# Optimization experiments

Hardware: AMD Instinct MI355X
Metric: run time of the kernel (lower is better)

The kernel has to match this reference:

```python
import jax, jax.numpy as jnp
import numpy as np

B, T, V, E, H = 64, 512, 50000, 256, 512
UNK_IDX = 1


def setup_inputs() -> dict:
    key = jax.random.key(0)
    ks = jax.random.split(key, 12)
    ids = jax.random.randint(ks[0], (B, T), 0, V)
    unk_mask = jax.random.uniform(ks[1], (B, T)) < 0.05
    enc_input = jnp.where(unk_mask, UNK_IDX, ids)
    lens = jnp.sort(jax.random.randint(ks[2], (B,), 256, T + 1))[::-1]
    seq_lens = lens.at[0].set(T)
    u = lambda k, sh: jax.random.uniform(k, sh, jnp.float32, -0.02, 0.02)
    emb_table = jax.random.normal(ks[3], (V, E), jnp.float32) * 0.1
    # torch gate order i,f,g,o; bias = b_ih + b_hh with forget-gate slice = 1.0 each -> 2.0 combined
    def bias(k):
        b = jnp.zeros((4 * H,), jnp.float32)
        return b.at[H:2 * H].set(2.0)
    return {
        "enc_input": enc_input,
        "seq_lens": seq_lens,
        "emb_table": emb_table,
        "Wih_f": u(ks[4], (4 * H, E)), "Whh_f": u(ks[5], (4 * H, H)), "b_f": bias(ks[6]),
        "Wih_b": u(ks[7], (4 * H, E)), "Whh_b": u(ks[8], (4 * H, H)), "b_b": bias(ks[9]),
        "Wp": u(ks[10], (E, 2 * H)) * 2.0, "bp": jnp.zeros((E,), jnp.float32),
    }


def _lstm_dir(x, mask, Wih, Whh, b, reverse):
    # x: [T,B,D], mask: [T,B] bool. Packed-sequence semantics: state frozen and
    # output zeroed at padded steps; reverse scan starts at t=len-1 per sequence.
    Bsz = x.shape[1]
    h0 = jnp.zeros((Bsz, H), x.dtype)
    c0 = jnp.zeros((Bsz, H), x.dtype)

    def step(carry, inp):
        h, c = carry
        x_t, m = inp
        g = x_t @ Wih.T + h @ Whh.T + b
        i, f, gg, o = jnp.split(g, 4, axis=-1)
        c_new = jax.nn.sigmoid(f) * c + jax.nn.sigmoid(i) * jnp.tanh(gg)
        h_new = jax.nn.sigmoid(o) * jnp.tanh(c_new)
        mm = m[:, None]
        h = jnp.where(mm, h_new, h)
        c = jnp.where(mm, c_new, c)
        return (h, c), jnp.where(mm, h_new, 0.0)

    (hT, cT), outs = jax.lax.scan(step, (h0, c0), (x, mask), reverse=reverse)
    return outs, hT, cT


def _bilstm(embedded, mask_tb, Wih_f, Whh_f, b_f, Wih_b, Whh_b, b_b):
    x = jnp.swapaxes(embedded, 0, 1)  # [T,B,E]
    of, hf, cf = _lstm_dir(x, mask_tb, Wih_f, Whh_f, b_f, reverse=False)
    ob, hb, cb = _lstm_dir(x, mask_tb, Wih_b, Whh_b, b_b, reverse=True)
    h = jnp.swapaxes(jnp.concatenate([of, ob], axis=-1), 0, 1)  # [B,T,2H]
    h_n = jnp.stack([hf, hb])  # [2,B,H]
    c_n = jnp.stack([cf, cb])
    return h, h_n, c_n


def reference(enc_input, seq_lens, emb_table, Wih_f, Whh_f, b_f, Wih_b, Whh_b, b_b, Wp, bp):
    valid = jnp.arange(T)[None, :] < seq_lens[:, None]  # [B,T]
    mask_tb = valid.T  # [T,B]
    embedded = emb_table[enc_input]  # [B,T,E]
    h, h_n, c_n = _bilstm(embedded, mask_tb, Wih_f, Whh_f, b_f, Wih_b, Whh_b, b_b)

    # vectorized OOV branch: replace UNK embeddings with proj of neighbor states
    is_unk = (enc_input == UNK_IDX) & valid  # [B,T]
    fwd_ctx = jnp.pad(h[:, :-1, :H], ((0, 0), (1, 0), (0, 0)))  # h[i,j-1,:H], 0 at j=0
    next_valid = (jnp.arange(T)[None, :] + 1) < seq_lens[:, None]
    bwd_ctx = jnp.pad(h[:, 1:, H:], ((0, 0), (0, 1), (0, 0))) * next_valid[..., None]
    unk_emb = jnp.concatenate([fwd_ctx, bwd_ctx], axis=-1)  # [B,T,2H]
    new_emb = unk_emb @ Wp.T + bp  # [B,T,E]
    embedded = jnp.where(is_unk[..., None], new_emb, embedded)

    h, h_n, c_n = _bilstm(embedded, mask_tb, Wih_f, Whh_f, b_f, Wih_b, Whh_b, b_b)
    return h, h_n, c_n
```

## Files before the change

kernel.cpp:

```cpp
#include <hip/hip_runtime.h>
#include <hip/hip_bf16.h>
#include <stdint.h>

typedef __attribute__((ext_vector_type(8))) short short8;
typedef __attribute__((ext_vector_type(4))) float f32x4;
typedef __attribute__((ext_vector_type(4))) unsigned int u32x4;

static __device__ __forceinline__ unsigned short f2b(float x) {
  union { float f; unsigned u; } v; v.f = x;
  unsigned r = (v.u + 0x7FFFu + ((v.u >> 16) & 1u)) >> 16;
  return (unsigned short)r;
}
static __device__ __forceinline__ float sigm(float x) { return 1.0f / (1.0f + __expf(-x)); }
static __device__ __forceinline__ float tanh_(float x) { return 2.0f / (1.0f + __expf(-2.0f * x)) - 1.0f; }

#define WS_EMB   0u
#define WS_WHH   16777216u
#define WS_WIH   20971520u
#define WS_WPB   23068672u
#define WS_SYNC  23592960u
#define WS_HEXS1 (WS_SYNC + 0u)
#define WS_HEXS2 (WS_SYNC + 262144u)
#define WS_HEXF1 (WS_SYNC + 524288u)
#define WS_HEXF2 (WS_SYNC + 786432u)
#define WS_CNTS1 (WS_SYNC + 1048576u)
#define WS_CNTS2 (WS_SYNC + 1052672u)
#define WS_CNTF1 (WS_SYNC + 1056768u)
#define WS_CNTF2 (WS_SYNC + 1060864u)
#define WS_REG1  (WS_SYNC + 1064960u)
#define WS_REG2  (WS_SYNC + 1065472u)
#define WS_SYNC_SPAN 1065984u

__global__ void prep(const float* __restrict__ wihf, const float* __restrict__ whhf,
                     const float* __restrict__ wihb, const float* __restrict__ whhb,
                     const float* __restrict__ wp,
                     unsigned short* __restrict__ wih_bf, unsigned short* __restrict__ whh_bf,
                     unsigned short* __restrict__ wp_bf) {
  int i = blockIdx.x * 256 + threadIdx.x;
  int stride = gridDim.x * 256;
  for (int k = i; k < 2048 * 512; k += stride) { whh_bf[k] = f2b(whhf[k]); whh_bf[2048 * 512 + k] = f2b(whhb[k]); }
  for (int k = i; k < 2048 * 256; k += stride) { wih_bf[k] = f2b(wihf[k]); wih_bf[2048 * 256 + k] = f2b(wihb[k]); }
  for (int k = i; k < 256 * 1024; k += stride) { wp_bf[k] = f2b(wp[k]); }
}

__global__ void gather(const int* __restrict__ enc, const float* __restrict__ tab,
                       unsigned short* __restrict__ emb) {
  for (int tok = blockIdx.x; tok < 64 * 512; tok += gridDim.x) {
    int b = tok >> 9, t = tok & 511;
    int id = enc[tok];
    int e = threadIdx.x;
    emb[(size_t)(t * 64 + b) * 256 + e] = f2b(tab[(size_t)id * 256 + e]);
  }
}

template<int FAST>
static __device__ __forceinline__ void lstm_body(
    int d, int q, int g,
    const unsigned short* __restrict__ emb,
    const unsigned short* __restrict__ whh,
    const unsigned short* __restrict__ wih,
    const float* __restrict__ bf_, const float* __restrict__ bb_,
    const int* __restrict__ lens,
    char* __restrict__ hexS, char* __restrict__ hexF,
    unsigned int* __restrict__ myc,
    float* __restrict__ out_h, float* __restrict__ out_hn, float* __restrict__ out_cn,
    unsigned short* lds_h, float (*gbuf)[16][17], unsigned short (*hnew)[16])
{
  const int tid = threadIdx.x;
  const int wv = tid >> 6, lane = tid & 63;
  const int l15 = lane & 15, lhi = lane >> 4;

  short8 Bh[16], Bx[8];
  {
    const int row = wv * 512 + g * 16 + l15;
    const unsigned short* pw = whh + ((size_t)d * 2048 + row) * 512 + lhi * 8;
#pragma unroll
    for (int kk = 0; kk < 16; ++kk) Bh[kk] = *(const short8*)(pw + kk * 32);
    const unsigned short* px = wih + ((size_t)d * 2048 + row) * 256 + lhi * 8;
#pragma unroll
    for (int kk = 0; kk < 8; ++kk) Bx[kk] = *(const short8*)(px + kk * 32);
  }
  const float bias = (d ? bb_ : bf_)[wv * 512 + g * 16 + l15];

  const int cb = tid & 15, ch = tid >> 4;
  const int gb = q * 16 + cb;
  const int mylen = lens[gb];
  float c_st = 0.f, h_cy = 0.f;

  char* hexG = FAST ? (hexF + (d * 4 + q) * 32768) : hexS;

  for (int s = 0; s < 512; ++s) {
    const int t = d ? (511 - s) : s;
    const int p = s & 1;

    f32x4 acc0 = { bias, bias, bias, bias };
    f32x4 acc1 = { 0.f, 0.f, 0.f, 0.f };
    {
      const unsigned short* xa = emb + ((size_t)(t * 64 + q * 16 + l15)) * 256 + lhi * 8;
#pragma unroll
      for (int kk = 0; kk < 8; ++kk) {
        short8 a = *(const short8*)(xa + kk * 32);
        acc0 = __builtin_amdgcn_mfma_f32_16x16x32_bf16(a, Bx[kk], acc0, 0, 0, 0);
      }
    }

    if (s > 0) {
      const unsigned int tgt = 32u * (unsigned)s;
      if (lane == 0) {
        if (FAST) {
          for (;;) {
            unsigned c;
            asm volatile("global_load_dword %0, %1, off sc0\n\ts_waitcnt vmcnt(0)"
                         : "=v"(c) : "v"(myc) : "memory");
            if (c >= tgt) break;
            __builtin_amdgcn_s_sleep(1);
          }
        } else {
          while (__hip_atomic_load(myc, __ATOMIC_RELAXED, __HIP_MEMORY_SCOPE_AGENT) < tgt)
            __builtin_amdgcn_s_sleep(1);
        }
      }
    }

    u32x4 hv0, hv1, hv2, hv3;
    {
      const char* src = FAST
          ? hexG + p * 16384 + (tid & 15) * 1024 + (tid >> 4) * 64
          : hexG + ((size_t)(p * 2 + d) * 64 + q * 16 + (tid & 15)) * 1024 + (tid >> 4) * 64;
      if (FAST) {
        asm volatile(
          "global_load_dwordx4 %0, %4, off sc0\n\t"
          "global_load_dwordx4 %1, %4, off offset:16 sc0\n\t"
          "global_load_dwordx4 %2, %4, off offset:32 sc0\n\t"
          "global_load_dwordx4 %3, %4, off offset:48 sc0\n\t"
          "s_waitcnt vmcnt(0)"
          : "=&v"(hv0), "=&v"(hv1), "=&v"(hv2), "=&v"(hv3) : "v"(src) : "memory");
      } else {
        asm volatile(
          "global_load_dwordx4 %0, %4, off sc0 sc1\n\t"
          "global_load_dwordx4 %1, %4, off offset:16 sc0 sc1\n\t"
          "global_load_dwordx4 %2, %4, off offset:32 sc0 sc1\n\t"
          "global_load_dwordx4 %3, %4, off offset:48 sc0 sc1\n\t"
          "s_waitcnt vmcnt(0)"
          : "=&v"(hv0), "=&v"(hv1), "=&v"(hv2), "=&v"(hv3) : "v"(src) : "memory");
      }
    }
    __syncthreads();
    {
      const int row = tid & 15;
      const int qt = tid >> 4;
      const int swz = (row & 7) << 4;
      char* base = (char*)lds_h + row * 1024;
      *(u32x4*)(base + ((qt * 64 +  0) ^ swz)) = hv0;
      *(u32x4*)(base + ((qt * 64 + 16) ^ swz)) = hv1;
      *(u32x4*)(base + ((qt * 64 + 32) ^ swz)) = hv2;
      *(u32x4*)(base + ((qt * 64 + 48) ^ swz)) = hv3;
    }
    __syncthreads();

    {
      const int rb0 = l15 * 1024 + lhi * 16;
      const int swz = (l15 & 7) << 4;
#pragma unroll
      for (int kk = 0; kk < 16; kk += 2) {
        short8 a0 = *(const short8*)((const char*)lds_h + ((rb0 + kk * 64) ^ swz));
        short8 a1 = *(const short8*)((const char*)lds_h + ((rb0 + (kk + 1) * 64) ^ swz));
        acc0 = __builtin_amdgcn_mfma_f32_16x16x32_bf16(a0, Bh[kk], acc0, 0, 0, 0);
        acc1 = __builtin_amdgcn_mfma_f32_16x16x32_bf16(a1, Bh[kk + 1], acc1, 0, 0, 0);
      }
    }
    f32x4 acc = acc0 + acc1;

#pragma unroll
    for (int r = 0; r < 4; ++r) gbuf[wv][l15][lhi * 4 + r] = acc[r];
    __syncthreads();

    float hn_out; bool m;
    {
      float gi = gbuf[0][ch][cb], gf = gbuf[1][ch][cb], gg = gbuf[2][ch][cb], go = gbuf[3][ch][cb];
      float cn_ = sigm(gf) * c_st + sigm(gi) * tanh_(gg);
      float hn_ = sigm(go) * tanh_(cn_);
      m = (t < mylen);
      c_st = m ? cn_ : c_st;
      h_cy = m ? hn_ : h_cy;
      hn_out = m ? hn_ : 0.f;
      hnew[cb][ch] = f2b(h_cy);
    }
    __syncthreads();

    if (wv == 0) {
      unsigned long long v = ((const unsigned long long*)hnew)[lane];
      char* dst = FAST
          ? hexG + ((s + 1) & 1) * 16384 + (lane >> 2) * 1024 + g * 32 + (lane & 3) * 8
          : hexG + ((size_t)(((s + 1) & 1) * 2 + d) * 64 + q * 16 + (lane >> 2)) * 1024 + g * 32 + (lane & 3) * 8;
      if (FAST) {
        asm volatile("global_store_dwordx2 %0, %1, off sc0" :: "v"(dst), "v"(v) : "memory");
        asm volatile("s_waitcnt vmcnt(0)" ::: "memory");
        if (lane == 0)
          __hip_atomic_fetch_add(myc, 1u, __ATOMIC_RELAXED, __HIP_MEMORY_SCOPE_WORKGROUP);
      } else {
        asm volatile("global_store_dwordx2 %0, %1, off sc0 sc1" :: "v"(dst), "v"(v) : "memory");
        asm volatile("s_waitcnt vmcnt(0)" ::: "memory");
        if (lane == 0)
          __hip_atomic_fetch_add(myc, 1u, __ATOMIC_RELAXED, __HIP_MEMORY_SCOPE_AGENT);
      }
    }

    out_h[((size_t)gb * 512 + t) * 1024 + d * 512 + g * 16 + ch] = hn_out;
    if (s == 511) {
      size_t o = ((size_t)d * 64 + gb) * 512 + g * 16 + ch;
      out_hn[o] = h_cy;
      out_cn[o] = c_st;
    }
  }
}

__global__ __launch_bounds__(256, 1) void lstm(
    const unsigned short* __restrict__ emb, const unsigned short* __restrict__ whh,
    const unsigned short* __restrict__ wih,
    const float* __restrict__ bf_, const float* __restrict__ bb_,
    const int* __restrict__ lens,
    char* __restrict__ hexS, char* __restrict__ hexF,
    unsigned int* __restrict__ cntS, unsigned int* __restrict__ cntF,
    unsigned int* __restrict__ reg,
    float* __restrict__ out_h, float* __restrict__ out_hn, float* __restrict__ out_cn)
{
  __shared__ __align__(16) unsigned short lds_h[16 * 512];
  __shared__ float gbuf[4][16][17];
  __shared__ __align__(8) unsigned short hnew[16][16];
  __shared__ int sh[4];

  const int tid = threadIdx.x;
  if (tid == 0) {
    unsigned xcd = 0;
    asm volatile("s_getreg_b32 %0, hwreg(HW_REG_XCC_ID)" : "=s"(xcd));
    xcd &= 7u;
    unsigned slot = __hip_atomic_fetch_add(&reg[xcd], 1u, __ATOMIC_RELAXED, __HIP_MEMORY_SCOPE_AGENT);
    unsigned v[8];
    for (;;) {
      unsigned sm = 0;
#pragma unroll
      for (int i = 0; i < 8; ++i) {
        v[i] = __hip_atomic_load(&reg[i], __ATOMIC_RELAXED, __HIP_MEMORY_SCOPE_AGENT);
        sm += v[i];
      }
      if (sm == 256u) break;
      __builtin_amdgcn_s_sleep(8);
    }
    bool clean = (slot < 32u);
    for (int i = 0; i < 8; ++i) clean = clean && (v[i] == 32u);
    if (clean) { sh[0] = 1; sh[1] = (int)(xcd >> 2); sh[2] = (int)(xcd & 3); sh[3] = (int)slot; }
    else {
      int bid = blockIdx.x;
      sh[0] = 0; sh[1] = bid >> 7; sh[2] = (bid >> 5) & 3; sh[3] = bid & 31;
    }
  }
  __syncthreads();
  const int fast = sh[0], d = sh[1], q = sh[2], g = sh[3];
  unsigned int* myc = (fast ? cntF : cntS) + (d * 4 + q) * 128;

  if (fast)
    lstm_body<1>(d, q, g, emb, whh, wih, bf_, bb_, lens, hexS, hexF, myc,
                 out_h, out_hn, out_cn, lds_h, gbuf, hnew);
  else
    lstm_body<0>(d, q, g, emb, whh, wih, bf_, bb_, lens, hexS, hexF, myc,
                 out_h, out_hn, out_cn, lds_h, gbuf, hnew);
}

__global__ __launch_bounds__(256, 1) void unkproj(
    const int* __restrict__ enc, const int* __restrict__ lens,
    const float* __restrict__ h1,
    const unsigned short* __restrict__ wpb,
    const float* __restrict__ bp,
    unsigned short* __restrict__ emb)
{
  const int base = blockIdx.x * 16;
  const int tid = threadIdx.x;
  const int wv = tid >> 6, lane = tid & 63;
  const int l15 = lane & 15, lhi = lane >> 4;

  const int tokA = base + l15;
  const int bA = tokA >> 9, tA = tokA & 511;
  const bool unkA = (enc[tokA] == 1) && (tA < lens[bA]);
  if (!__any(unkA)) return;

  const bool fok = (tA > 0), bok = (tA < 511);
  const float* fptr = h1 + ((size_t)bA * 512 + (fok ? tA - 1 : 0)) * 1024;
  const float* bptr = h1 + ((size_t)bA * 512 + (bok ? tA + 1 : 0)) * 1024 + 512;

  f32x4 acc[4] = { {0,0,0,0}, {0,0,0,0}, {0,0,0,0}, {0,0,0,0} };

#pragma unroll 4
  for (int kk = 0; kk < 16; ++kk) {
    const int k = kk * 32 + lhi * 8;
    short8 a;
    if (fok) {
      f32x4 lo = *(const f32x4*)(fptr + k);
      f32x4 hi = *(const f32x4*)(fptr + k + 4);
#pragma unroll
      for (int j = 0; j < 4; ++j) { a[j] = (short)f2b(lo[j]); a[4 + j] = (short)f2b(hi[j]); }
    } else {
      a = short8{0,0,0,0,0,0,0,0};
    }
#pragma unroll
    for (int nt = 0; nt < 4; ++nt) {
      short8 bf = *(const short8*)(wpb + (size_t)(wv * 64 + nt * 16 + l15) * 1024 + k);
      acc[nt] = __builtin_amdgcn_mfma_f32_16x16x32_bf16(a, bf, acc[nt], 0, 0, 0);
    }
  }
#pragma unroll 4
  for (int kk = 0; kk < 16; ++kk) {
    const int k = kk * 32 + lhi * 8;
    short8 a;
    if (bok) {
      f32x4 lo = *(const f32x4*)(bptr + k);
      f32x4 hi = *(const f32x4*)(bptr + k + 4);
#pragma unroll
      for (int j = 0; j < 4; ++j) { a[j] = (short)f2b(lo[j]); a[4 + j] = (short)f2b(hi[j]); }
    } else {
      a = short8{0,0,0,0,0,0,0,0};
    }
#pragma unroll
    for (int nt = 0; nt < 4; ++nt) {
      short8 bf = *(const short8*)(wpb + (size_t)(wv * 64 + nt * 16 + l15) * 1024 + 512 + k);
      acc[nt] = __builtin_amdgcn_mfma_f32_16x16x32_bf16(a, bf, acc[nt], 0, 0, 0);
    }
  }

#pragma unroll
  for (int r = 0; r < 4; ++r) {
    int tok = base + lhi * 4 + r;
    int b = tok >> 9, t = tok & 511;
    if (enc[tok] == 1 && t < lens[b]) {
#pragma unroll
      for (int nt = 0; nt < 4; ++nt) {
        int e = wv * 64 + nt * 16 + l15;
        emb[(size_t)(t * 64 + b) * 256 + e] = f2b(acc[nt][r] + bp[e]);
      }
    }
  }
}

extern "C" void kernel_launch(void* const* d_in, const int* in_sizes, int n_in,
                              void* d_out, int out_size, void* d_ws, size_t ws_size,
                              hipStream_t stream) {
  (void)in_sizes; (void)n_in; (void)out_size; (void)ws_size;
  const int*   enc  = (const int*)d_in[0];
  const int*   lens = (const int*)d_in[1];
  const float* tab  = (const float*)d_in[2];
  const float* wihf = (const float*)d_in[3];
  const float* whhf = (const float*)d_in[4];
  const float* bf_  = (const float*)d_in[5];
  const float* wihb = (const float*)d_in[6];
  const float* whhb = (const float*)d_in[7];
  const float* bb_  = (const float*)d_in[8];
  const float* wp   = (const float*)d_in[9];
  const float* bp   = (const float*)d_in[10];

  char* ws = (char*)d_ws;
  unsigned short* emb    = (unsigned short*)(ws + WS_EMB);
  unsigned short* whh_bf = (unsigned short*)(ws + WS_WHH);
  unsigned short* wih_bf = (unsigned short*)(ws + WS_WIH);
  unsigned short* wp_bf  = (unsigned short*)(ws + WS_WPB);

  float* out_h  = (float*)d_out;
  float* out_hn = out_h + (size_t)64 * 512 * 1024;
  float* out_cn = out_hn + 2 * 64 * 512;

  hipMemsetAsync(ws + WS_SYNC, 0, WS_SYNC_SPAN, stream);

  prep<<<2048, 256, 0, stream>>>(wihf, whhf, wihb, whhb, wp, wih_bf, whh_bf, wp_bf);
  gather<<<4096, 256, 0, stream>>>(enc, tab, emb);

  lstm<<<256, 256, 0, stream>>>(emb, whh_bf, wih_bf, bf_, bb_, lens,
                                ws + WS_HEXS1, ws + WS_HEXF1,
                                (unsigned int*)(ws + WS_CNTS1), (unsigned int*)(ws + WS_CNTF1),
                                (unsigned int*)(ws + WS_REG1),
                                out_h, out_hn, out_cn);
  unkproj<<<2048, 256, 0, stream>>>(enc, lens, out_h, wp_bf, bp, emb);
  lstm<<<256, 256, 0, stream>>>(emb, whh_bf, wih_bf, bf_, bb_, lens,
                                ws + WS_HEXS2, ws + WS_HEXF2,
                                (unsigned int*)(ws + WS_CNTS2), (unsigned int*)(ws + WS_CNTF2),
                                (unsigned int*)(ws + WS_REG2),
                                out_h, out_hn, out_cn);
}
```

Measured before the change: 3.414 ms.

## Halve LSTM block count, doubling hidden slice per block with per-block step flags

The persistent bidirectional LSTM kernel now runs 128 blocks of 512 threads, each owning 32 hidden units (8 waves), instead of 256 blocks of 256 threads with 16 units. The cross-block step barrier changes from an atomic counter to per-block step flags, which lanes poll in parallel with a wave-wide vote. Hidden-state exchange uses wider 16-byte stores and fewer loads per thread, and a watchdog limit is added to the spin loops. The aim is to cut the number of participants in each per-step global synchronisation and shorten the serial latency chain. In exchange each block does twice the MFMA work per step on a single CU, so per-step compute latency may grow.

```diff
diff --git a/kernel.cpp b/kernel.cpp
--- a/kernel.cpp
+++ b/kernel.cpp
@@ -19,17 +19,19 @@
 #define WS_WIH   20971520u
 #define WS_WPB   23068672u
 #define WS_SYNC  23592960u
-#define WS_HEXS1 (WS_SYNC + 0u)
-#define WS_HEXS2 (WS_SYNC + 262144u)
-#define WS_HEXF1 (WS_SYNC + 524288u)
-#define WS_HEXF2 (WS_SYNC + 786432u)
-#define WS_CNTS1 (WS_SYNC + 1048576u)
-#define WS_CNTS2 (WS_SYNC + 1052672u)
-#define WS_CNTF1 (WS_SYNC + 1056768u)
-#define WS_CNTF2 (WS_SYNC + 1060864u)
-#define WS_REG1  (WS_SYNC + 1064960u)
-#define WS_REG2  (WS_SYNC + 1065472u)
-#define WS_SYNC_SPAN 1065984u
+#define WS_HEXF1 (WS_SYNC + 0u)
+#define WS_HEXF2 (WS_SYNC + 262144u)
+#define WS_HEXS1 (WS_SYNC + 524288u)
+#define WS_HEXS2 (WS_SYNC + 786432u)
+#define WS_FLGF1 (WS_SYNC + 1048576u)
+#define WS_FLGF2 (WS_SYNC + 1049088u)
+#define WS_FLGS1 (WS_SYNC + 1049600u)
+#define WS_FLGS2 (WS_SYNC + 1050112u)
+#define WS_REG1  (WS_SYNC + 1050624u)
+#define WS_REG2  (WS_SYNC + 1051136u)
+#define WS_SYNC_SPAN 1051648u
+
+#define WD_LIMIT (1u << 17)
 
 __global__ void prep(const float* __restrict__ wihf, const float* __restrict__ whhf,
                      const float* __restrict__ wihb, const float* __restrict__ whhb,
@@ -61,18 +63,18 @@
     const unsigned short* __restrict__ wih,
     const float* __restrict__ bf_, const float* __restrict__ bb_,
     const int* __restrict__ lens,
-    char* __restrict__ hexS, char* __restrict__ hexF,
-    unsigned int* __restrict__ myc,
+    char* __restrict__ hexG, unsigned int* __restrict__ flg,
     float* __restrict__ out_h, float* __restrict__ out_hn, float* __restrict__ out_cn,
-    unsigned short* lds_h, float (*gbuf)[16][17], unsigned short (*hnew)[16])
+    unsigned short* lds_h, float (*gbuf)[32][17], unsigned short (*hnew)[40])
 {
   const int tid = threadIdx.x;
   const int wv = tid >> 6, lane = tid & 63;
   const int l15 = lane & 15, lhi = lane >> 4;
+  const int gt = wv >> 1, hs = wv & 1;
 
   short8 Bh[16], Bx[8];
+  const int row = gt * 512 + g * 32 + hs * 16 + l15;
   {
-    const int row = wv * 512 + g * 16 + l15;
     const unsigned short* pw = whh + ((size_t)d * 2048 + row) * 512 + lhi * 8;
 #pragma unroll
     for (int kk = 0; kk < 16; ++kk) Bh[kk] = *(const short8*)(pw + kk * 32);
@@ -80,15 +82,13 @@
 #pragma unroll
     for (int kk = 0; kk < 8; ++kk) Bx[kk] = *(const short8*)(px + kk * 32);
   }
-  const float bias = (d ? bb_ : bf_)[wv * 512 + g * 16 + l15];
+  const float bias = (d ? bb_ : bf_)[row];
 
   const int cb = tid & 15, ch = tid >> 4;
   const int gb = q * 16 + cb;
   const int mylen = lens[gb];
   float c_st = 0.f, h_cy = 0.f;
 
-  char* hexG = FAST ? (hexF + (d * 4 + q) * 32768) : hexS;
-
   for (int s = 0; s < 512; ++s) {
     const int t = d ? (511 - s) : s;
     const int p = s & 1;
@@ -105,56 +105,45 @@
     }
 
     if (s > 0) {
-      const unsigned int tgt = 32u * (unsigned)s;
-      if (lane == 0) {
-        if (FAST) {
-          for (;;) {
-            unsigned c;
-            asm volatile("global_load_dword %0, %1, off sc0\n\ts_waitcnt vmcnt(0)"
-                         : "=v"(c) : "v"(myc) : "memory");
-            if (c >= tgt) break;
-            __builtin_amdgcn_s_sleep(1);
-          }
-        } else {
-          while (__hip_atomic_load(myc, __ATOMIC_RELAXED, __HIP_MEMORY_SCOPE_AGENT) < tgt)
-            __builtin_amdgcn_s_sleep(1);
-        }
-      }
-    }
-
-    u32x4 hv0, hv1, hv2, hv3;
-    {
-      const char* src = FAST
-          ? hexG + p * 16384 + (tid & 15) * 1024 + (tid >> 4) * 64
-          : hexG + ((size_t)(p * 2 + d) * 64 + q * 16 + (tid & 15)) * 1024 + (tid >> 4) * 64;
-      if (FAST) {
+      const unsigned int tgt = (unsigned)s;
+      const unsigned int* fp = flg + (lane & 15);
+      for (unsigned it = 0;; ++it) {
+        unsigned f;
+        if (FAST)
+          asm volatile("global_load_dword %0, %1, off sc0\n\ts_waitcnt vmcnt(0)"
+                       : "=v"(f) : "v"(fp) : "memory");
+        else
+          asm volatile("global_load_dword %0, %1, off sc0 sc1\n\ts_waitcnt vmcnt(0)"
+                       : "=v"(f) : "v"(fp) : "memory");
+        if (__all((int)(f >= tgt))) break;
+        if (it > WD_LIMIT) break;
+        __builtin_amdgcn_s_sleep(1);
+      }
+    }
+
+    u32x4 hv0, hv1;
+    {
+      const char* src = hexG + p * 16384 + (tid >> 5) * 1024 + (tid & 31) * 32;
+      if (FAST)
         asm volatile(
-          "global_load_dwordx4 %0, %4, off sc0\n\t"
-          "global_load_dwordx4 %1, %4, off offset:16 sc0\n\t"
-          "global_load_dwordx4 %2, %4, off offset:32 sc0\n\t"
-          "global_load_dwordx4 %3, %4, off offset:48 sc0\n\t"
+          "global_load_dwordx4 %0, %2, off sc0\n\t"
+          "global_load_dwordx4 %1, %2, off offset:16 sc0\n\t"
           "s_waitcnt vmcnt(0)"
-          : "=&v"(hv0), "=&v"(hv1), "=&v"(hv2), "=&v"(hv3) : "v"(src) : "memory");
-      } else {
+          : "=&v"(hv0), "=&v"(hv1) : "v"(src) : "memory");
+      else
         asm volatile(
-          "global_load_dwordx4 %0, %4, off sc0 sc1\n\t"
-          "global_load_dwordx4 %1, %4, off offset:16 sc0 sc1\n\t"
-          "global_load_dwordx4 %2, %4, off offset:32 sc0 sc1\n\t"
-          "global_load_dwordx4 %3, %4, off offset:48 sc0 sc1\n\t"
+          "global_load_dwordx4 %0, %2, off sc0 sc1\n\t"
+          "global_load_dwordx4 %1, %2, off offset:16 sc0 sc1\n\t"
           "s_waitcnt vmcnt(0)"
-          : "=&v"(hv0), "=&v"(hv1), "=&v"(hv2), "=&v"(hv3) : "v"(src) : "memory");
-      }
-    }
-    __syncthreads();
-    {
-      const int row = tid & 15;
-      const int qt = tid >> 4;
-      const int swz = (row & 7) << 4;
-      char* base = (char*)lds_h + row * 1024;
-      *(u32x4*)(base + ((qt * 64 +  0) ^ swz)) = hv0;
-      *(u32x4*)(base + ((qt * 64 + 16) ^ swz)) = hv1;
-      *(u32x4*)(base + ((qt * 64 + 32) ^ swz)) = hv2;
-      *(u32x4*)(base + ((qt * 64 + 48) ^ swz)) = hv3;
+          : "=&v"(hv0), "=&v"(hv1) : "v"(src) : "memory");
+    }
+    {
+      const int row16 = tid >> 5;
+      const int off = (tid & 31) * 32;
+      const int swz = (row16 & 7) << 4;
+      char* base = (char*)lds_h + row16 * 1024;
+      *(u32x4*)(base + ((off) ^ swz)) = hv0;
+      *(u32x4*)(base + ((off + 16) ^ swz)) = hv1;
     }
     __syncthreads();
 
@@ -172,15 +161,15 @@
     f32x4 acc = acc0 + acc1;
 
 #pragma unroll
-    for (int r = 0; r < 4; ++r) gbuf[wv][l15][lhi * 4 + r] = acc[r];
+    for (int r = 0; r < 4; ++r) gbuf[gt][hs * 16 + l15][lhi * 4 + r] = acc[r];
     __syncthreads();
 
-    float hn_out; bool m;
+    float hn_out;
     {
       float gi = gbuf[0][ch][cb], gf = gbuf[1][ch][cb], gg = gbuf[2][ch][cb], go = gbuf[3][ch][cb];
       float cn_ = sigm(gf) * c_st + sigm(gi) * tanh_(gg);
       float hn_ = sigm(go) * tanh_(cn_);
-      m = (t < mylen);
+      bool m = (t < mylen);
       c_st = m ? cn_ : c_st;
       h_cy = m ? hn_ : h_cy;
       hn_out = m ? hn_ : 0.f;
@@ -189,45 +178,52 @@
     __syncthreads();
 
     if (wv == 0) {
-      unsigned long long v = ((const unsigned long long*)hnew)[lane];
-      char* dst = FAST
-          ? hexG + ((s + 1) & 1) * 16384 + (lane >> 2) * 1024 + g * 32 + (lane & 3) * 8
-          : hexG + ((size_t)(((s + 1) & 1) * 2 + d) * 64 + q * 16 + (lane >> 2)) * 1024 + g * 32 + (lane & 3) * 8;
+      const int prow = lane >> 2, c = lane & 3;
+      const char* hrow = (const char*)hnew + prow * 80 + c * 16;
+      unsigned long long a0 = *(const unsigned long long*)(hrow);
+      unsigned long long a1 = *(const unsigned long long*)(hrow + 8);
+      u32x4 v; v[0] = (unsigned)a0; v[1] = (unsigned)(a0 >> 32);
+      v[2] = (unsigned)a1; v[3] = (unsigned)(a1 >> 32);
+      char* dst = hexG + (p ^ 1) * 16384 + prow * 1024 + g * 64 + c * 16;
       if (FAST) {
-        asm volatile("global_store_dwordx2 %0, %1, off sc0" :: "v"(dst), "v"(v) : "memory");
-        asm volatile("s_waitcnt vmcnt(0)" ::: "memory");
-        if (lane == 0)
-          __hip_atomic_fetch_add(myc, 1u, __ATOMIC_RELAXED, __HIP_MEMORY_SCOPE_WORKGROUP);
+        asm volatile("global_store_dwordx4 %0, %1, off sc0\n\ts_waitcnt vmcnt(0)"
+                     :: "v"(dst), "v"(v) : "memory");
+        if (lane == 0) {
+          unsigned fv = (unsigned)(s + 1);
+          asm volatile("global_store_dword %0, %1, off sc0" :: "v"(flg + g), "v"(fv) : "memory");
+        }
       } else {
-        asm volatile("global_store_dwordx2 %0, %1, off sc0 sc1" :: "v"(dst), "v"(v) : "memory");
-        asm volatile("s_waitcnt vmcnt(0)" ::: "memory");
-        if (lane == 0)
-          __hip_atomic_fetch_add(myc, 1u, __ATOMIC_RELAXED, __HIP_MEMORY_SCOPE_AGENT);
-      }
-    }
-
-    out_h[((size_t)gb * 512 + t) * 1024 + d * 512 + g * 16 + ch] = hn_out;
+        asm volatile("global_store_dwordx4 %0, %1, off sc0 sc1\n\ts_waitcnt vmcnt(0)"
+                     :: "v"(dst), "v"(v) : "memory");
+        if (lane == 0) {
+          unsigned fv = (unsigned)(s + 1);
+          asm volatile("global_store_dword %0, %1, off sc0 sc1" :: "v"(flg + g), "v"(fv) : "memory");
+        }
+      }
+    }
+
+    out_h[((size_t)gb * 512 + t) * 1024 + d * 512 + g * 32 + ch] = hn_out;
     if (s == 511) {
-      size_t o = ((size_t)d * 64 + gb) * 512 + g * 16 + ch;
+      size_t o = ((size_t)d * 64 + gb) * 512 + g * 32 + ch;
       out_hn[o] = h_cy;
       out_cn[o] = c_st;
     }
   }
 }
 
-__global__ __launch_bounds__(256, 1) void lstm(
+__global__ __launch_bounds__(512, 1) void lstm(
     const unsigned short* __restrict__ emb, const unsigned short* __restrict__ whh,
     const unsigned short* __restrict__ wih,
     const float* __restrict__ bf_, const float* __restrict__ bb_,
     const int* __restrict__ lens,
-    char* __restrict__ hexS, char* __restrict__ hexF,
-    unsigned int* __restrict__ cntS, unsigned int* __restrict__ cntF,
+    char* __restrict__ hexF, char* __restrict__ hexS,
+    unsigned int* __restrict__ flgF, unsigned int* __restrict__ flgS,
     unsigned int* __restrict__ reg,
     float* __restrict__ out_h, float* __restrict__ out_hn, float* __restrict__ out_cn)
 {
   __shared__ __align__(16) unsigned short lds_h[16 * 512];
-  __shared__ float gbuf[4][16][17];
-  __shared__ __align__(8) unsigned short hnew[16][16];
+  __shared__ float gbuf[4][32][17];
+  __shared__ __align__(8) unsigned short hnew[16][40];
   __shared__ int sh[4];
 
   const int tid = threadIdx.x;
@@ -237,33 +233,33 @@
     xcd &= 7u;
     unsigned slot = __hip_atomic_fetch_add(&reg[xcd], 1u, __ATOMIC_RELAXED, __HIP_MEMORY_SCOPE_AGENT);
     unsigned v[8];
-    for (;;) {
+    bool done = false;
+    for (unsigned it = 0; it <= WD_LIMIT; ++it) {
       unsigned sm = 0;
 #pragma unroll
       for (int i = 0; i < 8; ++i) {
         v[i] = __hip_atomic_load(&reg[i], __ATOMIC_RELAXED, __HIP_MEMORY_SCOPE_AGENT);
         sm += v[i];
       }
-      if (sm == 256u) break;
+      if (sm == 128u) { done = true; break; }
       __builtin_amdgcn_s_sleep(8);
     }
-    bool clean = (slot < 32u);
-    for (int i = 0; i < 8; ++i) clean = clean && (v[i] == 32u);
-    if (clean) { sh[0] = 1; sh[1] = (int)(xcd >> 2); sh[2] = (int)(xcd & 3); sh[3] = (int)slot; }
-    else {
-      int bid = blockIdx.x;
-      sh[0] = 0; sh[1] = bid >> 7; sh[2] = (bid >> 5) & 3; sh[3] = bid & 31;
-    }
+    bool clean = done && (slot < 16u);
+    if (done) for (int i = 0; i < 8; ++i) clean = clean && (v[i] == 16u);
+    if (clean) { sh[0] = 1; sh[1] = (int)xcd; sh[2] = (int)slot; }
+    else       { sh[0] = 0; sh[1] = (int)(blockIdx.x >> 4); sh[2] = (int)(blockIdx.x & 15); }
   }
   __syncthreads();
-  const int fast = sh[0], d = sh[1], q = sh[2], g = sh[3];
-  unsigned int* myc = (fast ? cntF : cntS) + (d * 4 + q) * 128;
+  const int fast = sh[0], grp = sh[1], g = sh[2];
+  const int d = grp >> 2, q = grp & 3;
+  char* hexG = (fast ? hexF : hexS) + grp * 32768;
+  unsigned int* flg = (fast ? flgF : flgS) + grp * 16;
 
   if (fast)
-    lstm_body<1>(d, q, g, emb, whh, wih, bf_, bb_, lens, hexS, hexF, myc,
+    lstm_body<1>(d, q, g, emb, whh, wih, bf_, bb_, lens, hexG, flg,
                  out_h, out_hn, out_cn, lds_h, gbuf, hnew);
   else
-    lstm_body<0>(d, q, g, emb, whh, wih, bf_, bb_, lens, hexS, hexF, myc,
+    lstm_body<0>(d, q, g, emb, whh, wih, bf_, bb_, lens, hexG, flg,
                  out_h, out_hn, out_cn, lds_h, gbuf, hnew);
 }
 
@@ -372,15 +368,15 @@
   prep<<<2048, 256, 0, stream>>>(wihf, whhf, wihb, whhb, wp, wih_bf, whh_bf, wp_bf);
   gather<<<4096, 256, 0, stream>>>(enc, tab, emb);
 
-  lstm<<<256, 256, 0, stream>>>(emb, whh_bf, wih_bf, bf_, bb_, lens,
-                                ws + WS_HEXS1, ws + WS_HEXF1,
-                                (unsigned int*)(ws + WS_CNTS1), (unsigned int*)(ws + WS_CNTF1),
+  lstm<<<128, 512, 0, stream>>>(emb, whh_bf, wih_bf, bf_, bb_, lens,
+                                ws + WS_HEXF1, ws + WS_HEXS1,
+                                (unsigned int*)(ws + WS_FLGF1), (unsigned int*)(ws + WS_FLGS1),
                                 (unsigned int*)(ws + WS_REG1),
                                 out_h, out_hn, out_cn);
   unkproj<<<2048, 256, 0, stream>>>(enc, lens, out_h, wp_bf, bp, emb);
-  lstm<<<256, 256, 0, stream>>>(emb, whh_bf, wih_bf, bf_, bb_, lens,
-                                ws + WS_HEXS2, ws + WS_HEXF2,
-                                (unsigned int*)(ws + WS_CNTS2), (unsigned int*)(ws + WS_CNTF2),
+  lstm<<<128, 512, 0, stream>>>(emb, whh_bf, wih_bf, bf_, bb_, lens,
+                                ws + WS_HEXF2, ws + WS_HEXS2,
+                                (unsigned int*)(ws + WS_FLGF2), (unsigned int*)(ws + WS_FLGS2),
                                 (unsigned int*)(ws + WS_REG2),
                                 out_h, out_hn, out_cn);
 }
```

Measured after the change: 3.743 ms. 9.6% more time.
